# Kernel tuning notes

Hardware: AMD Instinct MI355X
Metric: run time of the kernel (lower is better)

Reference implementation:

```python
import jax, jax.numpy as jnp
import numpy as np

N = 1000        # genomes
S = 32          # samples
M = 2_000_000   # total genes
K = 100_000     # sequences (contigs)


def setup_inputs() -> dict:
    key = jax.random.key(0)
    k1, k2, k3, k4, k5 = jax.random.split(key, 5)
    A = jax.random.normal(k1, (N, S), dtype=jnp.float32)          # log-abundance
    B = jax.random.uniform(k2, (N, S), dtype=jnp.float32)         # log-PTR in [0,1]
    pos = jax.random.uniform(k3, (M,), dtype=jnp.float32)         # gene position in [0,1]
    genome_idx = jax.random.randint(k4, (M,), 0, N)               # one-hot column of `members`
    seq_idx = jax.random.randint(k5, (M,), 0, K)                  # row of `gene_to_seq`
    return {"A": A, "B": B, "pos": pos, "genome_idx": genome_idx, "seq_idx": seq_idx}


def reference(A, B, pos, genome_idx, seq_idx):
    # G = members @ A + 1 - dists @ B  ==  A[g] + 1 - pos * B[g] per gene  -> [M, S]
    G = A[genome_idx] + 1.0 - pos[:, None] * B[genome_idx]
    # E @ exp(G): sum exp(G) over genes belonging to each sequence -> [K, S]
    return jax.ops.segment_sum(jnp.exp(G), seq_idx, num_segments=K)
```

## Files before the change

### kernel.cpp

```cpp
#include <hip/hip_runtime.h>
#include <hip/hip_bf16.h>


#define CHUNK 8192
#define NBMAX 1024
#define CAPLG 12
#define CAP   (1 << CAPLG)
#define SCAP  3072

__device__ inline float fast_exp2(float x) {
    float r;
    asm("v_exp_f32 %0, %1" : "=v"(r) : "v"(x));
    return r;
}

__global__ __launch_bounds__(256) void prep_kernel(
    const float* __restrict__ A, const float* __restrict__ B,
    unsigned* __restrict__ AB2p, int* __restrict__ gcur, int NS)
{
    const int i = blockIdx.x * 256 + threadIdx.x;
    if (i < NBMAX) gcur[i] = 0;
    if (i >= NS) return;
    const float a2 = (A[i] + 1.0f) * 1.44269504f;
    const float b2 = B[i] * (1.44269504f / 32768.0f);
    const _Float16 ha = (_Float16)a2;
    const unsigned short ua = __builtin_bit_cast(unsigned short, ha);
    unsigned bb = __float_as_uint(b2);
    bb = (bb + 0x7FFFu + ((bb >> 16) & 1u)) & 0xFFFF0000u;
    AB2p[i] = (unsigned)ua | bb;
}

__global__ __launch_bounds__(1024) void partition_kernel(
    const float* __restrict__ pos, const int* __restrict__ gidx,
    const int* __restrict__ sidx, int* __restrict__ gcur,
    unsigned* __restrict__ payload, int M, int NB)
{
    __shared__ int h[NBMAX];
    __shared__ int pfx[NBMAX];
    __shared__ int cur[NBMAX];
    __shared__ int wsum[16];
    __shared__ unsigned stg_p[CHUNK];
    __shared__ unsigned short stg_b[CHUNK];
    const int t = threadIdx.x, blk = blockIdx.x;
    const int i0 = blk * CHUNK;
    const int n = min(CHUNK, M - i0);

    h[t] = 0;
    __syncthreads();
    for (int j = t; j < n; j += 1024) atomicAdd(&h[sidx[i0 + j] >> 7], 1);
    __syncthreads();

    {
        const int v = h[t];
        int incl = v;
#pragma unroll
        for (int d = 1; d < 64; d <<= 1) {
            const int x = __shfl_up(incl, d);
            if ((t & 63) >= d) incl += x;
        }
        if ((t & 63) == 63) wsum[t >> 6] = incl;
        __syncthreads();
        if (t < 16) {
            const int wv = wsum[t];
            int winc = wv;
#pragma unroll
            for (int d = 1; d < 16; d <<= 1) {
                const int x = __shfl_up(winc, d, 16);
                if (t >= d) winc += x;
            }
            wsum[t] = winc - wv;
        }
        __syncthreads();
        const int ex = wsum[t >> 6] + incl - v;
        pfx[t] = ex;
        cur[t] = ex;
    }
    __syncthreads();

    for (int j = t; j < n; j += 1024) {
        const int sx = sidx[i0 + j];
        const int b = sx >> 7;
        const float p = pos[i0 + j];
        int q = (int)fmaf(p, 32768.0f, 0.5f);
        q = min(q, 32767);
        const unsigned pl = (unsigned)(sx & 127)
                          | ((unsigned)gidx[i0 + j] << 7)
                          | ((unsigned)q << 17);
        const int d = atomicAdd(&cur[b], 1);
        stg_p[d] = pl;
        stg_b[d] = (unsigned short)b;
    }
    __syncthreads();

    if (t < NB) {
        const int hc = h[t];
        int dst = t << CAPLG;
        if (hc > 0) dst += atomicAdd(&gcur[t], hc);
        cur[t] = dst;
    }
    __syncthreads();

    for (int tt = t; tt < n; tt += 1024) {
        const int b = stg_b[tt];
        const int r = cur[b] + (tt - pfx[b]);
        if ((r >> CAPLG) == b) payload[r] = stg_p[tt];
    }
}

#define GENE(w, dst)                                                        \
    {                                                                       \
        const float qf = (float)((w) >> 17);                                \
        const unsigned voff = ((w) & 0x1FF80u) | lane4;                     \
        const unsigned ab = *(const unsigned*)((const char*)AB2p + voff);   \
        float a2v;                                                          \
        asm("v_cvt_f32_f16 %0, %1" : "=v"(a2v) : "v"(ab));                  \
        dst += fast_exp2(fmaf(-qf, __int_as_float(ab & 0xFFFF0000u), a2v)); \
    }

__global__ __launch_bounds__(512) void fused_reduce_kernel(
    const unsigned* __restrict__ AB2p, const unsigned* __restrict__ payload,
    const int* __restrict__ gcur, float* __restrict__ out, int K)
{
    __shared__ unsigned sorted[SCAP];
    __shared__ int h[64];
    __shared__ int pfx[64];
    const int t = threadIdx.x;
    const int bkt = blockIdx.x >> 1;
    const int sp  = blockIdx.x & 1;
    const int s32 = t & 31;
    const int half = (t >> 5) & 1;
    const int wv = t >> 6;
    const unsigned lane4 = (unsigned)(s32 << 2);
    const int start = bkt << CAPLG;
    const int n = min(gcur[bkt], CAP);

    if (t < 64) h[t] = 0;
    __syncthreads();

    unsigned r[8];
    int rk[8];
#pragma unroll
    for (int u = 0; u < 8; u++) {
        const int idx = t + u * 512;
        rk[u] = -1;
        if (idx < n) {
            const unsigned w = payload[start + idx];
            if ((int)((w >> 6) & 1u) == sp) {
                r[u] = w;
                rk[u] = atomicAdd(&h[w & 63], 1);
            }
        }
    }
    __syncthreads();

    if (t < 64) {
        const int v = h[t];
        int incl = v;
#pragma unroll
        for (int d = 1; d < 64; d <<= 1) {
            const int x = __shfl_up(incl, d);
            if (t >= d) incl += x;
        }
        pfx[t] = incl - v;
    }
    __syncthreads();

#pragma unroll
    for (int u = 0; u < 8; u++)
        if (rk[u] >= 0) {
            const int d = pfx[r[u] & 63] + rk[u];
            if (d < SCAP) sorted[d] = r[u];
        }
    __syncthreads();

    const int seqbase = (bkt << 7) + (sp << 6) + (wv << 3);
    for (int q = 0; q < 8; q++) {
        const int ls = (wv << 3) + q;
        int i = pfx[ls];
        const int e = min(i + h[ls], SCAP);
        float a0 = 0.0f, a1 = 0.0f;
        for (; i + 3 < e; i += 4) {
            const int ix = i + (half << 1);
            const unsigned w0 = sorted[ix];
            const unsigned w1 = sorted[ix + 1];
            GENE(w0, a0); GENE(w1, a1);
        }
        for (; i + 1 < e; i += 2) {
            const unsigned w0 = sorted[i + half];
            GENE(w0, a0);
        }
        if (i < e && half == 0) {
            const unsigned w0 = sorted[i];
            GENE(w0, a0);
        }
        float acc = a0 + a1;
        acc += __shfl_xor(acc, 32);
        const int seq = seqbase + q;
        if (half == 0 && seq < K) out[(seq << 5) + s32] = acc;
    }
}

__global__ __launch_bounds__(256) void scatter_exp_fallback(
    const float* __restrict__ A, const float* __restrict__ B,
    const float* __restrict__ pos, const int* __restrict__ gidx,
    const int* __restrict__ sidx, float* __restrict__ out, int M)
{
    const int lane = threadIdx.x & 31;
    int group = (int)((blockIdx.x * blockDim.x + threadIdx.x) >> 5);
    const int stride = (int)((gridDim.x * blockDim.x) >> 5);
    for (int g = group; g < M; g += stride) {
        const int gi = gidx[g];
        const int si = sidx[g];
        const float p = pos[g];
        const float a = A[(gi << 5) + lane];
        const float b = B[(gi << 5) + lane];
        atomicAdd(&out[(si << 5) + lane], __expf(fmaf(-p, b, a + 1.0f)));
    }
}

extern "C" void kernel_launch(void* const* d_in, const int* in_sizes, int n_in,
                              void* d_out, int out_size, void* d_ws, size_t ws_size,
                              hipStream_t stream)
{
    const float* A    = (const float*)d_in[0];
    const float* B    = (const float*)d_in[1];
    const float* pos  = (const float*)d_in[2];
    const int*   gidx = (const int*)d_in[3];
    const int*   sidx = (const int*)d_in[4];
    float*       out  = (float*)d_out;

    const int M  = in_sizes[2];
    const int NS = in_sizes[0];
    const int N  = NS / 32;
    const int K  = out_size / 32;
    const int NB = (K + 127) >> 7;
    const int NBLK = (M + CHUNK - 1) / CHUNK;

    char* ws = (char*)d_ws;
    size_t off = 0;
    int* gcur = (int*)(ws + off);       off += (size_t)NBMAX * sizeof(int);
    off = (off + 255) & ~(size_t)255;
    unsigned* AB2p = (unsigned*)(ws + off); off += (size_t)N * 32 * sizeof(unsigned);
    off = (off + 255) & ~(size_t)255;
    unsigned* payload = (unsigned*)(ws + off);
    const size_t need = off + ((size_t)NB << CAPLG) * sizeof(unsigned);

    const bool packable = (NB <= NBMAX) && (K <= NBMAX * 128) && (N <= 1024)
                       && (M / (NB > 0 ? NB : 1) <= CAP / 4 * 3);
    if (!packable || ws_size < need) {
        hipMemsetAsync(d_out, 0, (size_t)out_size * sizeof(float), stream);
        scatter_exp_fallback<<<8192, 256, 0, stream>>>(A, B, pos, gidx, sidx, out, M);
        return;
    }

    const int prep_grid = (max(NS, NBMAX) + 255) / 256;
    prep_kernel     <<<prep_grid, 256, 0, stream>>>(A, B, AB2p, gcur, NS);
    partition_kernel<<<NBLK, 1024, 0, stream>>>(pos, gidx, sidx, gcur, payload, M, NB);
    fused_reduce_kernel<<<NB * 2, 512, 0, stream>>>(AB2p, payload, gcur, out, K);
}
```

Measured before the change: 60.10 us.

## Keep partition payloads in registers and process two samples per lane in reduce

The partition kernel now reads sidx/pos/gidx once, holding each element's packed payload, bucket and within-bucket rank in registers across the prefix scan. This replaces the second global read pass and the second round of shared atomics. The reduce kernel remaps each wavefront so that 16 lanes each handle two samples through 8-byte AB2p loads, letting four genes be processed per wave step. Out-of-range genes are masked to a large negative exponent instead of using tail branches, and results are written as float2. The cost is more register pressure from the 8-element arrays and some wasted lanes on short segments.

```diff
diff --git a/kernel.cpp b/kernel.cpp
--- a/kernel.cpp
+++ b/kernel.cpp
@@ -37,7 +37,7 @@
 {
     __shared__ int h[NBMAX];
     __shared__ int pfx[NBMAX];
-    __shared__ int cur[NBMAX];
+    __shared__ int dbase[NBMAX];
     __shared__ int wsum[16];
     __shared__ unsigned stg_p[CHUNK];
     __shared__ unsigned short stg_b[CHUNK];
@@ -47,7 +47,26 @@
 
     h[t] = 0;
     __syncthreads();
-    for (int j = t; j < n; j += 1024) atomicAdd(&h[sidx[i0 + j] >> 7], 1);
+
+    unsigned pl[8];
+    int bb[8], rk[8];
+#pragma unroll
+    for (int u = 0; u < 8; u++) {
+        const int j = t + u * 1024;
+        rk[u] = -1;
+        if (j < n) {
+            const int sx = sidx[i0 + j];
+            const int b = sx >> 7;
+            const float p = pos[i0 + j];
+            int q = (int)fmaf(p, 32768.0f, 0.5f);
+            q = min(q, 32767);
+            pl[u] = (unsigned)(sx & 127)
+                  | ((unsigned)gidx[i0 + j] << 7)
+                  | ((unsigned)q << 17);
+            bb[u] = b;
+            rk[u] = atomicAdd(&h[b], 1);
+        }
+    }
     __syncthreads();
 
     {
@@ -71,66 +90,48 @@
             wsum[t] = winc - wv;
         }
         __syncthreads();
-        const int ex = wsum[t >> 6] + incl - v;
-        pfx[t] = ex;
-        cur[t] = ex;
-    }
-    __syncthreads();
-
-    for (int j = t; j < n; j += 1024) {
-        const int sx = sidx[i0 + j];
-        const int b = sx >> 7;
-        const float p = pos[i0 + j];
-        int q = (int)fmaf(p, 32768.0f, 0.5f);
-        q = min(q, 32767);
-        const unsigned pl = (unsigned)(sx & 127)
-                          | ((unsigned)gidx[i0 + j] << 7)
-                          | ((unsigned)q << 17);
-        const int d = atomicAdd(&cur[b], 1);
-        stg_p[d] = pl;
-        stg_b[d] = (unsigned short)b;
-    }
+        pfx[t] = wsum[t >> 6] + incl - v;
+    }
+    __syncthreads();
+
+#pragma unroll
+    for (int u = 0; u < 8; u++)
+        if (rk[u] >= 0) {
+            const int d = pfx[bb[u]] + rk[u];
+            stg_p[d] = pl[u];
+            stg_b[d] = (unsigned short)bb[u];
+        }
     __syncthreads();
 
     if (t < NB) {
         const int hc = h[t];
         int dst = t << CAPLG;
         if (hc > 0) dst += atomicAdd(&gcur[t], hc);
-        cur[t] = dst;
+        dbase[t] = dst;
     }
     __syncthreads();
 
     for (int tt = t; tt < n; tt += 1024) {
         const int b = stg_b[tt];
-        const int r = cur[b] + (tt - pfx[b]);
+        const int r = dbase[b] + (tt - pfx[b]);
         if ((r >> CAPLG) == b) payload[r] = stg_p[tt];
     }
 }
-
-#define GENE(w, dst)                                                        \
-    {                                                                       \
-        const float qf = (float)((w) >> 17);                                \
-        const unsigned voff = ((w) & 0x1FF80u) | lane4;                     \
-        const unsigned ab = *(const unsigned*)((const char*)AB2p + voff);   \
-        float a2v;                                                          \
-        asm("v_cvt_f32_f16 %0, %1" : "=v"(a2v) : "v"(ab));                  \
-        dst += fast_exp2(fmaf(-qf, __int_as_float(ab & 0xFFFF0000u), a2v)); \
-    }
 
 __global__ __launch_bounds__(512) void fused_reduce_kernel(
     const unsigned* __restrict__ AB2p, const unsigned* __restrict__ payload,
     const int* __restrict__ gcur, float* __restrict__ out, int K)
 {
-    __shared__ unsigned sorted[SCAP];
+    __shared__ unsigned sorted[SCAP + 8];
     __shared__ int h[64];
     __shared__ int pfx[64];
     const int t = threadIdx.x;
     const int bkt = blockIdx.x >> 1;
     const int sp  = blockIdx.x & 1;
-    const int s32 = t & 31;
-    const int half = (t >> 5) & 1;
+    const int g4  = (t >> 4) & 3;
+    const int l16 = t & 15;
+    const unsigned lane8 = (unsigned)(l16 << 3);
     const int wv = t >> 6;
-    const unsigned lane4 = (unsigned)(s32 << 2);
     const int start = bkt << CAPLG;
     const int n = min(gcur[bkt], CAP);
 
@@ -173,31 +174,47 @@
         }
     __syncthreads();
 
+#define GPROC(gi, A0, A1)                                                     \
+    {                                                                         \
+        const unsigned w = sorted[gi];                                        \
+        const bool valid = (gi) < e;                                          \
+        const unsigned voff = (w & 0x1FF80u) | lane8;                         \
+        const uint2 ab = *(const uint2*)((const char*)AB2p + voff);           \
+        const float qf = (float)(w >> 17);                                    \
+        float fa0, fa1;                                                       \
+        asm("v_cvt_f32_f16 %0, %1" : "=v"(fa0) : "v"(ab.x));                  \
+        asm("v_cvt_f32_f16 %0, %1" : "=v"(fa1) : "v"(ab.y));                  \
+        float x0 = fmaf(-qf, __int_as_float(ab.x & 0xFFFF0000u), fa0);        \
+        float x1 = fmaf(-qf, __int_as_float(ab.y & 0xFFFF0000u), fa1);        \
+        x0 = valid ? x0 : -2000.0f;                                           \
+        x1 = valid ? x1 : -2000.0f;                                           \
+        A0 += fast_exp2(x0);                                                  \
+        A1 += fast_exp2(x1);                                                  \
+    }
+
     const int seqbase = (bkt << 7) + (sp << 6) + (wv << 3);
     for (int q = 0; q < 8; q++) {
         const int ls = (wv << 3) + q;
-        int i = pfx[ls];
-        const int e = min(i + h[ls], SCAP);
-        float a0 = 0.0f, a1 = 0.0f;
-        for (; i + 3 < e; i += 4) {
-            const int ix = i + (half << 1);
-            const unsigned w0 = sorted[ix];
-            const unsigned w1 = sorted[ix + 1];
-            GENE(w0, a0); GENE(w1, a1);
-        }
-        for (; i + 1 < e; i += 2) {
-            const unsigned w0 = sorted[i + half];
-            GENE(w0, a0);
-        }
-        if (i < e && half == 0) {
-            const unsigned w0 = sorted[i];
-            GENE(w0, a0);
-        }
-        float acc = a0 + a1;
-        acc += __shfl_xor(acc, 32);
+        const int i0 = pfx[ls];
+        const int e = min(i0 + h[ls], SCAP);
+        float a0 = 0.0f, a1 = 0.0f, b0 = 0.0f, b1 = 0.0f;
+        int i = i0;
+        for (; i + 4 < e; i += 8) {
+            GPROC(i + g4, a0, a1);
+            GPROC(i + 4 + g4, b0, b1);
+        }
+        for (; i < e; i += 4)
+            GPROC(i + g4, a0, a1);
+        float acc0 = a0 + b0, acc1 = a1 + b1;
+        acc0 += __shfl_xor(acc0, 16);
+        acc1 += __shfl_xor(acc1, 16);
+        acc0 += __shfl_xor(acc0, 32);
+        acc1 += __shfl_xor(acc1, 32);
         const int seq = seqbase + q;
-        if (half == 0 && seq < K) out[(seq << 5) + s32] = acc;
-    }
+        if ((t & 48) == 0 && seq < K)
+            *(float2*)&out[(seq << 5) + (l16 << 1)] = make_float2(acc0, acc1);
+    }
+#undef GPROC
 }
 
 __global__ __launch_bounds__(256) void scatter_exp_fallback(
```

New measurement: 57.27 us. 1.05x faster.
